# Optimization experiments

Hardware: AMD Instinct MI355X
Metric: run time of the kernel (lower is better)

## Reference

```python
import jax, jax.numpy as jnp
import numpy as np

NL, DM, DI, DS, DC, DR = 8, 512, 1024, 16, 4, 32  # layers, d_model, d_inner, d_state, d_conv, dt_rank
B_, F_, HW, PF, P = 8, 32, 160, 4, 16


def setup_inputs() -> dict:
    key = jax.random.key(0)
    ks = iter(jax.random.split(key, 64))
    def rn(shape, s=0.02):
        return jax.random.normal(next(ks), shape, jnp.float32) * s
    inp = {"x": jax.random.normal(next(ks), (B_, 1, F_, HW, HW), jnp.float32)}
    inp["patch_w"] = rn((P * P * PF * 1, DM)); inp["patch_b"] = jnp.zeros((DM,), jnp.float32)
    inp["in_proj_w"] = rn((NL, DM, 2 * DI))
    inp["conv_w"] = rn((NL, DI, DC), 0.2); inp["conv_b"] = jnp.zeros((NL, DI), jnp.float32)
    inp["xproj_w"] = rn((NL, DI, DR + 2 * DS))
    inp["dt_w"] = rn((NL, DR, DI)); inp["dt_bias"] = rn((NL, DI), 0.1)
    A0 = jnp.log(jnp.arange(1, DS + 1, dtype=jnp.float32))
    inp["A_log"] = jnp.tile(A0, (NL, DI, 1)); inp["D_skip"] = jnp.ones((NL, DI), jnp.float32)
    inp["conv_w_b"] = rn((NL, DI, DC), 0.2); inp["conv_b_b"] = jnp.zeros((NL, DI), jnp.float32)
    inp["xproj_w_b"] = rn((NL, DI, DR + 2 * DS))
    inp["dt_w_b"] = rn((NL, DR, DI)); inp["dt_bias_b"] = rn((NL, DI), 0.1)
    inp["A_log_b"] = jnp.tile(A0, (NL, DI, 1)); inp["D_skip_b"] = jnp.ones((NL, DI), jnp.float32)
    inp["out_proj_w"] = rn((NL, DI, DM))
    inp["ln1_g"] = jnp.ones((NL, DM), jnp.float32); inp["ln1_b"] = jnp.zeros((NL, DM), jnp.float32)
    inp["fc1_w"] = rn((NL, DM, 1024)); inp["fc1_b"] = jnp.zeros((NL, 1024), jnp.float32)
    inp["fc2_w"] = rn((NL, 1024, DM)); inp["fc2_b"] = jnp.zeros((NL, DM), jnp.float32)
    inp["ln2_g"] = jnp.ones((NL, DM), jnp.float32); inp["ln2_b"] = jnp.zeros((NL, DM), jnp.float32)
    return inp


def _ln(x, g, b):
    m = jnp.mean(x, -1, keepdims=True)
    v = jnp.mean(jnp.square(x - m), -1, keepdims=True)
    return (x - m) * jax.lax.rsqrt(v + 1e-5) * g + b


def _causal_conv(x, w, b):
    # x: (B, L, DI); depthwise causal conv over L, kernel DC, then SiLU
    xt = x.transpose(0, 2, 1)  # (B, DI, L)
    y = jax.lax.conv_general_dilated(xt, w[:, None, :], (1,), [(DC - 1, 0)],
                                     feature_group_count=DI,
                                     dimension_numbers=("NCH", "OIH", "NCH"))
    return jax.nn.silu(y + b[None, :, None]).transpose(0, 2, 1)


def _ssm(u, dt, A, Bm, Cm, Dv):
    # u, dt: (B, L, DI); A: (DI, DS); Bm, Cm: (B, L, DS); Dv: (DI,)
    def step(h, t):
        dt_t, B_t, C_t, u_t = t  # (B,DI),(B,DS),(B,DS),(B,DI)
        h = jnp.exp(dt_t[..., None] * A) * h + (dt_t * u_t)[..., None] * B_t[:, None, :]
        return h, jnp.einsum("bdn,bn->bd", h, C_t)
    h0 = jnp.zeros((u.shape[0], DI, DS), u.dtype)
    _, ys = jax.lax.scan(step, h0, (dt.swapaxes(0, 1), Bm.swapaxes(0, 1),
                                    Cm.swapaxes(0, 1), u.swapaxes(0, 1)))
    return ys.swapaxes(0, 1) + u * Dv


def _mamba_dir(xc, z, xp_w, dtw, dtb, a_log, dv):
    proj = xc @ xp_w  # (B, L, DR+2*DS)
    dti, Bm, Cm = jnp.split(proj, [DR, DR + DS], axis=-1)
    dt = jax.nn.softplus(dti @ dtw + dtb)
    y = _ssm(xc, dt, -jnp.exp(a_log), Bm, Cm, dv)
    return y * jax.nn.silu(z)


def reference(x, patch_w, patch_b, in_proj_w, conv_w, conv_b, xproj_w, dt_w, dt_bias,
              A_log, D_skip, conv_w_b, conv_b_b, xproj_w_b, dt_w_b, dt_bias_b,
              A_log_b, D_skip_b, out_proj_w, ln1_g, ln1_b, fc1_w, fc1_b,
              fc2_w, fc2_b, ln2_g, ln2_b):
    b, c, Ft, H, W = x.shape
    f, h, w = Ft // PF, H // P, W // P
    # Rearrange: b c (f pf) (h p1) (w p2) -> b (f h w) (p1 p2 pf c)
    xp = x.reshape(b, c, f, PF, h, P, w, P).transpose(0, 2, 4, 6, 5, 7, 3, 1)
    xt = xp.reshape(b, f * h * w, P * P * PF * c) @ patch_w + patch_b  # (B, 800, 512)
    outs = []
    for l in range(NL):
        xz = xt @ in_proj_w[l]
        xm, z = jnp.split(xz, 2, axis=-1)  # (B, L, DI) each
        yf = _mamba_dir(_causal_conv(xm, conv_w[l], conv_b[l]), z,
                        xproj_w[l], dt_w[l], dt_bias[l], A_log[l], D_skip[l])
        yb = _mamba_dir(_causal_conv(xm[:, ::-1], conv_w_b[l], conv_b_b[l]), z[:, ::-1],
                        xproj_w_b[l], dt_w_b[l], dt_bias_b[l], A_log_b[l], D_skip_b[l])
        y = (yf + yb[:, ::-1]) @ out_proj_w[l]
        xt = _ln(y, ln1_g[l], ln1_b[l]) + xt  # MambaLayer (dropout=eval identity) + residual
        m = jax.nn.gelu(xt @ fc1_w[l] + fc1_b[l], approximate=False) @ fc2_w[l] + fc2_b[l]
        xt = _ln(m, ln2_g[l], ln2_b[l]) + xt  # MlpChannel + residual
        outs.append(xt)
    return jnp.stack(outs)  # (NL, B, 800, 512); original returns this as a list
```

## Files before the change

### kernel.cpp

```cpp
#include <hip/hip_runtime.h>


typedef unsigned short u16;
typedef unsigned long long u64;
typedef short s16x8 __attribute__((ext_vector_type(8)));
typedef float f32x4 __attribute__((ext_vector_type(4)));

#define NSEG 10
#define SEGLEN 80

__device__ __forceinline__ float b2f(u16 u) {
    return __uint_as_float(((unsigned)u) << 16);
}
__device__ __forceinline__ u16 f2b(float f) {
    unsigned u = __float_as_uint(f);
    return (u16)((u + 0x7fffu + ((u >> 16) & 1u)) >> 16);
}
__device__ __forceinline__ float ldw(const void* p, size_t i, int bf) {
    return bf ? b2f(((const u16*)p)[i]) : ((const float*)p)[i];
}
__device__ __forceinline__ float4 ldw4(const void* p, size_t i, int bf) {
    if (bf) {
        ushort4 v = *(const ushort4*)((const u16*)p + i);
        return make_float4(b2f(v.x), b2f(v.y), b2f(v.z), b2f(v.w));
    }
    return *(const float4*)((const float*)p + i);
}

__device__ __forceinline__ int detect_bf(const void* w) {
    const u16* p = (const u16*)w;
    unsigned e = (p[threadIdx.x & 63] >> 7) & 0xFFu;
    u64 m = __ballot((e >= 0x60u) && (e <= 0x7Fu));
    return __popcll(m) >= 50 ? 1 : 0;
}

#if __has_builtin(__builtin_amdgcn_exp2f)
#define EXP2F(x) __builtin_amdgcn_exp2f(x)
#else
#define EXP2F(x) __expf((x) * 0.69314718055994531f)
#endif

template<int EPI>
__device__ __forceinline__ float epi_act(float x) {
    if (EPI == 2) {
        float t = __expf(-fabsf(x));
        return fmaxf(x, 0.f) + __logf(1.f + t);
    }
    if (EPI == 3) {
        float y = 0.7978845608f * fmaf(0.044715f * x, x * x, x);
        float e = __expf(fminf(2.f * y, 80.f));
        float th = (e - 1.f) / (e + 1.f);
        return 0.5f * x * (1.f + th);
    }
    return x;
}

__global__ __launch_bounds__(256) void transp_cvt(
    const void* __restrict__ src, u16* __restrict__ dst, int K, int N,
    const void* __restrict__ sniff)
{
    const int bf = detect_bf(sniff);
    __shared__ u16 tile[32][33];
    const int n0 = blockIdx.x * 32, k0 = blockIdx.y * 32;
    const size_t loff = (size_t)blockIdx.z * K * N;
    const int tx = threadIdx.x, ty = threadIdx.y;
    #pragma unroll
    for (int r = 0; r < 4; r++) {
        int ky = ty + r * 8;
        tile[ky][tx] = f2b(ldw(src, loff + (size_t)(k0 + ky) * N + n0 + tx, bf));
    }
    __syncthreads();
    #pragma unroll
    for (int r = 0; r < 4; r++) {
        int ny = ty + r * 8;
        dst[loff + (size_t)(n0 + ny) * K + k0 + tx] = tile[tx][ny];
    }
}

template<int EPI, bool OUTF, bool OUTB>
__global__ __launch_bounds__(256) void gemm_mfma(
    const u16* __restrict__ A, const u16* __restrict__ WT, size_t woff,
    const void* __restrict__ bias, size_t soff,
    float* __restrict__ Cf, u16* __restrict__ Cb,
    int M, int N, int K, const void* __restrict__ sniff)
{
    const int bf = detect_bf(sniff);
    __shared__ __align__(16) u16 As[128 * 32];
    __shared__ __align__(16) u16 Bs[128 * 32];
    const int tid = threadIdx.x;
    const int bm = blockIdx.y * 128, bn = blockIdx.x * 128;
    const int w = tid >> 6, lane = tid & 63;
    const int wm = (w >> 1) * 64, wn = (w & 1) * 64;
    const int lrow = lane & 15, q = lane >> 4;
    const u16* Wp = WT + woff;

    f32x4 acc[4][4];
    const f32x4 z4 = {0.f, 0.f, 0.f, 0.f};
    #pragma unroll
    for (int i = 0; i < 4; i++)
        #pragma unroll
        for (int j = 0; j < 4; j++) acc[i][j] = z4;

    for (int k0 = 0; k0 < K; k0 += 32) {
        if (k0) __syncthreads();
        #pragma unroll
        for (int c = 0; c < 2; c++) {
            int jj = tid + c * 256;
            int r = jj >> 2, kc = jj & 3;
            int kg = kc ^ ((r >> 1) & 3);
            int ra = bm + r; if (ra >= M) ra = M - 1;
            *(s16x8*)(As + r * 32 + kc * 8) =
                *(const s16x8*)(A + (size_t)ra * K + k0 + kg * 8);
            *(s16x8*)(Bs + r * 32 + kc * 8) =
                *(const s16x8*)(Wp + (size_t)(bn + r) * K + k0 + kg * 8);
        }
        __syncthreads();
        s16x8 af[4], bfr[4];
        #pragma unroll
        for (int mt = 0; mt < 4; mt++) {
            int m_ = wm + mt * 16 + lrow;
            af[mt] = *(const s16x8*)(As + m_ * 32 + ((q ^ ((m_ >> 1) & 3)) << 3));
        }
        #pragma unroll
        for (int nt = 0; nt < 4; nt++) {
            int n_ = wn + nt * 16 + lrow;
            bfr[nt] = *(const s16x8*)(Bs + n_ * 32 + ((q ^ ((n_ >> 1) & 3)) << 3));
        }
        #pragma unroll
        for (int mt = 0; mt < 4; mt++)
            #pragma unroll
            for (int nt = 0; nt < 4; nt++)
                acc[mt][nt] = __builtin_amdgcn_mfma_f32_16x16x32_bf16(
                    af[mt], bfr[nt], acc[mt][nt], 0, 0, 0);
    }

    float bv[4] = {0.f, 0.f, 0.f, 0.f};
    if (EPI >= 1) {
        #pragma unroll
        for (int nt = 0; nt < 4; nt++)
            bv[nt] = ldw(bias, soff + (size_t)(bn + wn + nt * 16 + lrow), bf);
    }
    #pragma unroll
    for (int mt = 0; mt < 4; mt++) {
        #pragma unroll
        for (int nt = 0; nt < 4; nt++) {
            int n = bn + wn + nt * 16 + lrow;
            #pragma unroll
            for (int reg = 0; reg < 4; reg++) {
                int m = bm + wm + mt * 16 + q * 4 + reg;
                if (m < M) {
                    float v = epi_act<EPI>(acc[mt][nt][reg] + bv[nt]);
                    if (OUTF) Cf[(size_t)m * N + n] = v;
                    if (OUTB) Cb[(size_t)m * N + n] = f2b(v);
                }
            }
        }
    }
}

template<int EPI>
__device__ __forceinline__ void gemm_body(
    const float* __restrict__ A,
    const void* __restrict__ Bw, size_t boff,
    const void* __restrict__ bias, size_t soff,
    float* __restrict__ C, int N, int K, int lda, int ldb, int ldc, int bf)
{
    __shared__ float As[16][68];
    __shared__ float Bs[16][68];
    const int tid = threadIdx.x;
    const int bm = blockIdx.y * 64;
    const int bn = blockIdx.x * 64;
    const int arow = tid >> 2, acol = (tid & 3) << 2;
    const int brow = tid >> 4, bcol = (tid & 15) << 2;
    const int ty = tid >> 4, tx = tid & 15;
    float acc[4][4] = {};

    const float* aptr = A + (size_t)(bm + arow) * lda + acol;
    const size_t bidx0 = boff + (size_t)brow * ldb + bn + bcol;

    for (int k0 = 0; k0 < K; k0 += 16) {
        float4 av = *(const float4*)(aptr + k0);
        float4 bvv = ldw4(Bw, bidx0 + (size_t)k0 * ldb, bf);
        As[acol + 0][arow] = av.x;
        As[acol + 1][arow] = av.y;
        As[acol + 2][arow] = av.z;
        As[acol + 3][arow] = av.w;
        Bs[brow][bcol + 0] = bvv.x;
        Bs[brow][bcol + 1] = bvv.y;
        Bs[brow][bcol + 2] = bvv.z;
        Bs[brow][bcol + 3] = bvv.w;
        __syncthreads();
        #pragma unroll
        for (int kk = 0; kk < 16; kk++) {
            float4 a4 = *(const float4*)&As[kk][ty << 2];
            float4 b4 = *(const float4*)&Bs[kk][tx << 2];
            float ar[4] = {a4.x, a4.y, a4.z, a4.w};
            float br[4] = {b4.x, b4.y, b4.z, b4.w};
            #pragma unroll
            for (int i = 0; i < 4; i++)
                #pragma unroll
                for (int j = 0; j < 4; j++)
                    acc[i][j] = fmaf(ar[i], br[j], acc[i][j]);
        }
        __syncthreads();
    }

    float bv4[4] = {0.f, 0.f, 0.f, 0.f};
    if (EPI >= 1) {
        float4 bb = ldw4(bias, soff + (size_t)(bn + (tx << 2)), bf);
        bv4[0] = bb.x; bv4[1] = bb.y; bv4[2] = bb.z; bv4[3] = bb.w;
    }
    #pragma unroll
    for (int i = 0; i < 4; i++) {
        float4 o;
        o.x = epi_act<EPI>(acc[i][0] + bv4[0]);
        o.y = epi_act<EPI>(acc[i][1] + bv4[1]);
        o.z = epi_act<EPI>(acc[i][2] + bv4[2]);
        o.w = epi_act<EPI>(acc[i][3] + bv4[3]);
        *(float4*)(C + (size_t)(bm + (ty << 2) + i) * ldc + bn + (tx << 2)) = o;
    }
}

template<int EPI>
__global__ __launch_bounds__(256) void gemm_dual(
    const float* __restrict__ A0, const float* __restrict__ A1,
    const void* __restrict__ Bw0, size_t boff0,
    const void* __restrict__ Bw1, size_t boff1,
    const void* __restrict__ bias0, size_t sof0,
    const void* __restrict__ bias1, size_t sof1,
    float* __restrict__ C0, float* __restrict__ C1,
    int N, int K, int lda, int ldb, int ldc,
    const void* __restrict__ sniff)
{
    const int bf = detect_bf(sniff);
    if (blockIdx.z == 0)
        gemm_body<EPI>(A0, Bw0, boff0, bias0, sof0, C0, N, K, lda, ldb, ldc, bf);
    else
        gemm_body<EPI>(A1, Bw1, boff1, bias1, sof1, C1, N, K, lda, ldb, ldc, bf);
}

__global__ __launch_bounds__(256) void xproj_splitk(
    const float* __restrict__ A0, const float* __restrict__ A1,
    const void* __restrict__ Bw0, size_t boff0,
    const void* __restrict__ Bw1, size_t boff1,
    float* __restrict__ P, int Mc, const void* __restrict__ sniff)
{
    const int bf = detect_bf(sniff);
    const int dir = blockIdx.z;
    const float* A = dir ? A1 : A0;
    const void* Bw = dir ? Bw1 : Bw0;
    const size_t boff = dir ? boff1 : boff0;

    __shared__ float As[16][68];
    __shared__ float Bs[16][68];
    const int tid = threadIdx.x;
    const int bm = blockIdx.y * 64;
    const int kbase = blockIdx.x * 128;
    const int arow = tid >> 2, acol = (tid & 3) << 2;
    const int brow = tid >> 4, bcol = (tid & 15) << 2;
    const int ty = tid >> 4, tx = tid & 15;
    float acc[4][4] = {};

    const float* aptr = A + (size_t)(bm + arow) * 1024 + kbase + acol;
    const size_t bidx0 = boff + (size_t)(kbase + brow) * 64 + bcol;

    for (int k0 = 0; k0 < 128; k0 += 16) {
        float4 av = *(const float4*)(aptr + k0);
        float4 bvv = ldw4(Bw, bidx0 + (size_t)k0 * 64, bf);
        As[acol + 0][arow] = av.x;
        As[acol + 1][arow] = av.y;
        As[acol + 2][arow] = av.z;
        As[acol + 3][arow] = av.w;
        Bs[brow][bcol + 0] = bvv.x;
        Bs[brow][bcol + 1] = bvv.y;
        Bs[brow][bcol + 2] = bvv.z;
        Bs[brow][bcol + 3] = bvv.w;
        __syncthreads();
        #pragma unroll
        for (int kk = 0; kk < 16; kk++) {
            float4 a4 = *(const float4*)&As[kk][ty << 2];
            float4 b4 = *(const float4*)&Bs[kk][tx << 2];
            float ar[4] = {a4.x, a4.y, a4.z, a4.w};
            float br[4] = {b4.x, b4.y, b4.z, b4.w};
            #pragma unroll
            for (int i = 0; i < 4; i++)
                #pragma unroll
                for (int j = 0; j < 4; j++)
                    acc[i][j] = fmaf(ar[i], br[j], acc[i][j]);
        }
        __syncthreads();
    }

    float* out = P + ((size_t)(blockIdx.x * 2 + dir) * Mc + bm) * 64;
    #pragma unroll
    for (int i = 0; i < 4; i++) {
        float4 o = {acc[i][0], acc[i][1], acc[i][2], acc[i][3]};
        *(float4*)(out + (size_t)((ty << 2) + i) * 64 + (tx << 2)) = o;
    }
}

__global__ __launch_bounds__(256) void xproj_reduce(
    const float* __restrict__ P, float* __restrict__ o0,
    float* __restrict__ o1, unsigned Md)
{
    const int dir = blockIdx.y;
    unsigned i = (blockIdx.x * 256 + threadIdx.x) * 4;
    const float* p = P + (size_t)dir * Md + i;
    float4 a = *(const float4*)p;
    #pragma unroll
    for (int kc = 1; kc < 8; kc++) {
        float4 bq = *(const float4*)(p + (size_t)kc * 2 * Md);
        a.x += bq.x; a.y += bq.y; a.z += bq.z; a.w += bq.w;
    }
    *(float4*)((dir ? o1 : o0) + i) = a;
}

__global__ __launch_bounds__(256) void im2col_patch(
    const void* __restrict__ x, size_t x0, u16* __restrict__ Pb,
    const void* __restrict__ sniff)
{
    const int bf = detect_bf(sniff);
    int idx = blockIdx.x * 256 + threadIdx.x;
    int p2 = idx & 15; int r = idx >> 4;
    int p1 = r & 15;  r >>= 4;
    int w = r % 10;   r /= 10;
    int h = r % 10;   r /= 10;
    int f = r & 7;    int b = r >> 3;
    int token = f * 100 + h * 10 + w;
    size_t xb = x0 + ((size_t)(b * 32 + f * 4) * 160 + h * 16 + p1) * 160
                   + (w * 16 + p2);
    ushort4 o;
    o.x = f2b(ldw(x, xb,         bf));
    o.y = f2b(ldw(x, xb + 25600, bf));
    o.z = f2b(ldw(x, xb + 51200, bf));
    o.w = f2b(ldw(x, xb + 76800, bf));
    *(ushort4*)(Pb + (size_t)(b * 800 + token) * 1024 + ((p1 * 16 + p2) << 2)) = o;
}

__global__ __launch_bounds__(256) void conv_dual(
    const float* __restrict__ xm,
    const void* __restrict__ cwF, size_t wFo,
    const void* __restrict__ cbF, size_t bFo,
    const void* __restrict__ cwB, size_t wBo,
    const void* __restrict__ cbB, size_t bBo,
    float* __restrict__ xcf, float* __restrict__ xcb,
    const void* __restrict__ sniff)
{
    const int bf = detect_bf(sniff);
    int idx = blockIdx.x * 256 + threadIdx.x;
    int d = idx & 1023;
    int bt = idx >> 10;
    int t = bt % 800, b = bt / 800;
    const float* base = xm + (size_t)b * 800 * 2048 + d;
    float v[7];
    #pragma unroll
    for (int j = 0; j < 7; j++) {
        int tt = t + j - 3;
        v[j] = (tt >= 0 && tt < 800) ? base[(size_t)tt * 2048] : 0.f;
    }
    float4 wf = ldw4(cwF, wFo + (size_t)d * 4, bf);
    float4 wb = ldw4(cwB, wBo + (size_t)d * 4, bf);
    float f = ldw(cbF, bFo + d, bf) + wf.x * v[0] + wf.y * v[1]
                                    + wf.z * v[2] + wf.w * v[3];
    float g = ldw(cbB, bBo + d, bf) + wb.x * v[6] + wb.y * v[5]
                                    + wb.z * v[4] + wb.w * v[3];
    xcf[(size_t)bt * 1024 + d] = f / (1.f + __expf(-f));
    xcb[(size_t)bt * 1024 + d] = g / (1.f + __expf(-g));
}

__device__ __forceinline__ float& scrf(float* s, unsigned i) {
    return s[(size_t)(i >> 10) * 2048 + (i & 1023)];
}

__device__ __forceinline__ void pow16(float q, float* e) {
    float q2 = q * q, q4 = q2 * q2, q8 = q4 * q4;
    e[0] = q;        e[1] = q2;       e[2] = q2 * q;   e[3] = q4;
    e[4] = q4 * q;   e[5] = q4 * q2;  e[6] = e[5] * q; e[7] = q8;
    e[8] = q8 * q;   e[9] = q8 * q2;  e[10] = e[9] * q; e[11] = q8 * q4;
    e[12] = e[11] * q; e[13] = e[11] * q2; e[14] = e[13] * q; e[15] = q8 * q8;
}

template<int DIR, int PASS, bool POW>
__device__ __forceinline__ void scan_seg_body(
    const float* u, const float* dt, const float* __restrict__ pr,
    const void* __restrict__ Al, size_t ao,
    const void* __restrict__ Dp, size_t dofs,
    float* y, float* scr, unsigned NSd, int b, int seg, int bf,
    float* lds)
{
    const int tid = threadIdx.x;
    const int d = blockIdx.x * 256 + tid;
    const long rb = (long)b * 800;
    constexpr int S = DIR ? -1 : 1;
    const int t0 = DIR ? 799 - seg * SEGLEN : seg * SEGLEN;

    for (int i = tid; i < 768; i += 256) {
        int tr = i >> 3, c4 = (i & 7) * 4;
        long tt = (long)t0 + (long)(S * tr);
        *(float4*)&lds[tr * 32 + c4] =
            *(const float4*)&pr[(rb + tt) * 64 + 32 + c4];
    }
    __syncthreads();

    float ac[16];
    #pragma unroll
    for (int n = 0; n < 16; n++)
        ac[n] = -__expf(ldw(Al, ao + (size_t)d * 16 + n, bf)) * 1.44269504f;
    const float ac0 = ac[0];
    const float Dv = (PASS == 3) ? ldw(Dp, dofs + d, bf) : 0.f;

    const unsigned sidx = ((unsigned)((b * 2 + DIR) * NSEG + seg) << 10) + d;
    float h[16];
    if (PASS == 3) {
        #pragma unroll
        for (int n = 0; n < 16; n++) h[n] = scrf(scr, (16 + n) * NSd + sidx);
    } else {
        #pragma unroll
        for (int n = 0; n < 16; n++) h[n] = 0.f;
    }
    float E[16]; float Q = 1.f;
    if (PASS == 1 && !POW) {
        #pragma unroll
        for (int n = 0; n < 16; n++) E[n] = 1.f;
    }

    const float* pdt = dt + (rb + t0) * 1024 + d;
    const float* pu  = u  + (rb + t0) * 1024 + d;
    float*       py  = y  + (rb + t0) * 1024 + d;

    float dA[8], uA[8], dB[8], uB_[8];
    #pragma unroll
    for (int j = 0; j < 8; j++) { dA[j] = pdt[S * j * 1024]; uA[j] = pu[S * j * 1024]; }
    pdt += S * 8192; pu += S * 8192;

    for (int it = 0; it < SEGLEN / 8; it++) {
        #pragma unroll
        for (int j = 0; j < 8; j++) { dB[j] = pdt[S * j * 1024]; uB_[j] = pu[S * j * 1024]; }
        pdt += S * 8192; pu += S * 8192;

        #pragma unroll
        for (int j = 0; j < 8; j++) {
            const float dtv = dA[j], uv = uA[j];
            const float du = dtv * uv;
            float e[16];
            if (POW) {
                float q = EXP2F(dtv * ac0);
                pow16(q, e);
                if (PASS == 1) Q *= q;
            } else {
                #pragma unroll
                for (int n = 0; n < 16; n++) e[n] = EXP2F(dtv * ac[n]);
                if (PASS == 1) {
                    #pragma unroll
                    for (int n = 0; n < 16; n++) E[n] *= e[n];
                }
            }
            const float* bcp = lds + (it * 8 + j) * 32;
            float bs[16];
            *(float4*)&bs[0]  = *(const float4*)&bcp[0];
            *(float4*)&bs[4]  = *(const float4*)&bcp[4];
            *(float4*)&bs[8]  = *(const float4*)&bcp[8];
            *(float4*)&bs[12] = *(const float4*)&bcp[12];
            #pragma unroll
            for (int n = 0; n < 16; n++) h[n] = e[n] * h[n] + du * bs[n];
            if (PASS == 3) {
                float cs[16];
                *(float4*)&cs[0]  = *(const float4*)&bcp[16];
                *(float4*)&cs[4]  = *(const float4*)&bcp[20];
                *(float4*)&cs[8]  = *(const float4*)&bcp[24];
                *(float4*)&cs[12] = *(const float4*)&bcp[28];
                float s0 = 0.f, s1 = 0.f, s2 = 0.f, s3 = 0.f;
                #pragma unroll
                for (int n = 0; n < 4; n++) {
                    s0 = fmaf(h[n],      cs[n],      s0);
                    s1 = fmaf(h[4 + n],  cs[4 + n],  s1);
                    s2 = fmaf(h[8 + n],  cs[8 + n],  s2);
                    s3 = fmaf(h[12 + n], cs[12 + n], s3);
                }
                py[S * j * 1024] = fmaf(uv, Dv, (s0 + s1) + (s2 + s3));
            }
        }
        if (PASS == 3) py += S * 8192;
        #pragma unroll
        for (int j = 0; j < 8; j++) { dA[j] = dB[j]; uA[j] = uB_[j]; }
    }

    if (PASS == 1) {
        if (POW) pow16(Q, E);
        #pragma unroll
        for (int n = 0; n < 16; n++) {
            scrf(scr, n * NSd + sidx)        = E[n];
            scrf(scr, (16 + n) * NSd + sidx) = h[n];
        }
    }
}

template<int PASS>
__global__ __launch_bounds__(256) void ssm_seg(
    const float* uF, const float* dtF, const float* __restrict__ pF,
    const float* uB, const float* dtB, const float* __restrict__ pB,
    const void* __restrict__ AlF, const void* __restrict__ AlB, size_t ao,
    const void* __restrict__ DF,  const void* __restrict__ DB,  size_t dofs,
    float* yF, float* yB, float* scr, unsigned NSd,
    const void* __restrict__ sniff)
{
    __shared__ float lds[96 * 32];
    const int bf = detect_bf(sniff);
    const int b = blockIdx.y;
    const int z = blockIdx.z;
    const int dir = z >= NSEG ? 1 : 0;
    const int seg = dir ? z - NSEG : z;
    const int d = blockIdx.x * 256 + threadIdx.x;

    const void* Al = dir ? AlB : AlF;
    float m0 = __expf(ldw(Al, ao + (size_t)d * 16 + 0, bf));
    bool okb = true;
    #pragma unroll
    for (int n = 1; n < 16; n++) {
        float mn = __expf(ldw(Al, ao + (size_t)d * 16 + n, bf));
        okb &= fabsf(mn - (n + 1) * m0) <= 1e-3f * (n + 1) * m0;
    }
    const bool ok = __all(okb) != 0;

    if (dir == 0) {
        if (ok) scan_seg_body<0, PASS, true >(uF, dtF, pF, AlF, ao, DF, dofs,
                                              yF, scr, NSd, b, seg, bf, lds);
        else    scan_seg_body<0, PASS, false>(uF, dtF, pF, AlF, ao, DF, dofs,
                                              yF, scr, NSd, b, seg, bf, lds);
    } else {
        if (ok) scan_seg_body<1, PASS, true >(uB, dtB, pB, AlB, ao, DB, dofs,
                                              yB, scr, NSd, b, seg, bf, lds);
        else    scan_seg_body<1, PASS, false>(uB, dtB, pB, AlB, ao, DB, dofs,
                                              yB, scr, NSd, b, seg, bf, lds);
    }
}

__global__ __launch_bounds__(256) void ssm_comb(float* scr, unsigned NSd)
{
    int idx = blockIdx.x * 256 + threadIdx.x;
    int d = idx & 1023;
    int n = (idx >> 10) & 15;
    int bdir = idx >> 14;
    float h = 0.f;
    for (int s = 0; s < NSEG; s++) {
        unsigned sidx = ((unsigned)(bdir * NSEG + s) << 10) + d;
        float Ev = scrf(scr, n * NSd + sidx);
        float He = scrf(scr, (16 + n) * NSd + sidx);
        scrf(scr, (16 + n) * NSd + sidx) = h;
        h = Ev * h + He;
    }
}

__global__ __launch_bounds__(256) void addcvt(
    const float* __restrict__ a, const float* __restrict__ b,
    const float* __restrict__ z, u16* __restrict__ o)
{
    int i = (blockIdx.x * 256 + threadIdx.x) * 4;
    int t = i >> 10, d = i & 1023;
    float4 va = *(const float4*)(a + i);
    float4 vb = *(const float4*)(b + i);
    float4 vz = *(const float4*)(z + (size_t)t * 2048 + 1024 + d);
    float s0 = vz.x / (1.f + __expf(-vz.x));
    float s1 = vz.y / (1.f + __expf(-vz.y));
    float s2 = vz.z / (1.f + __expf(-vz.z));
    float s3 = vz.w / (1.f + __expf(-vz.w));
    ushort4 r;
    r.x = f2b((va.x + vb.x) * s0); r.y = f2b((va.y + vb.y) * s1);
    r.z = f2b((va.z + vb.z) * s2); r.w = f2b((va.w + vb.w) * s3);
    *(ushort4*)(o + i) = r;
}

__global__ __launch_bounds__(256) void ln_residual(
    const float* __restrict__ Y, const void* __restrict__ g, size_t go,
    const void* __restrict__ bb, size_t bo,
    float* __restrict__ XT, u16* __restrict__ XTb, float* __restrict__ out,
    const void* __restrict__ sniff)
{
    const int bf = detect_bf(sniff);
    int wv = threadIdx.x >> 6, lane = threadIdx.x & 63;
    int token = blockIdx.x * 4 + wv;
    const float* y = Y + (size_t)token * 512;
    float v[8], s = 0.f, s2 = 0.f;
    #pragma unroll
    for (int j = 0; j < 8; j++) {
        v[j] = y[lane + j * 64];
        s += v[j]; s2 += v[j] * v[j];
    }
    #pragma unroll
    for (int off = 32; off >= 1; off >>= 1) {
        s  += __shfl_xor(s,  off, 64);
        s2 += __shfl_xor(s2, off, 64);
    }
    float mean = s * (1.f / 512.f);
    float var  = s2 * (1.f / 512.f) - mean * mean;
    float rs = rsqrtf(var + 1e-5f);
    float* xt = XT + (size_t)token * 512;
    #pragma unroll
    for (int j = 0; j < 8; j++) {
        int c = lane + j * 64;
        float val = (v[j] - mean) * rs * ldw(g, go + c, bf)
                  + ldw(bb, bo + c, bf) + xt[c];
        xt[c] = val;
        XTb[(size_t)token * 512 + c] = f2b(val);
        if (out) out[(size_t)token * 512 + c] = val;
    }
}

extern "C" void kernel_launch(void* const* d_in, const int* in_sizes, int n_in,
                              void* d_out, int out_size, void* d_ws, size_t ws_size,
                              hipStream_t stream)
{
    (void)in_sizes; (void)n_in; (void)out_size;
    const void* X      = d_in[0];
    const void* patchW = d_in[1];
    const void* patchB = d_in[2];
    const void* inW    = d_in[3];
    const void* convW  = d_in[4];
    const void* convBi = d_in[5];
    const void* xprojW = d_in[6];
    const void* dtW    = d_in[7];
    const void* dtBias = d_in[8];
    const void* Alog   = d_in[9];
    const void* Dsk    = d_in[10];
    const void* convWb = d_in[11];
    const void* convBb = d_in[12];
    const void* xprojWb= d_in[13];
    const void* dtWb   = d_in[14];
    const void* dtBiasb= d_in[15];
    const void* Alogb  = d_in[16];
    const void* Dskb   = d_in[17];
    const void* outW   = d_in[18];
    const void* ln1g   = d_in[19];
    const void* ln1b   = d_in[20];
    const void* fc1W   = d_in[21];
    const void* fc1B   = d_in[22];
    const void* fc2W   = d_in[23];
    const void* fc2B   = d_in[24];
    const void* ln2g   = d_in[25];
    const void* ln2b   = d_in[26];
    const void* SN     = patchW;

    const size_t IN_OFF  = 524288;
    const size_t OUT_OFF = 8912896;
    const size_t FC1_OFF = 13107200;
    const size_t FC2_OFF = 17301504;
    const size_t WB_FLOATS = 10747904;

    int nc = 1;
    auto need = [&](int Mc) {
        return (WB_FLOATS + (size_t)Mc * 8064 + 16384) * 4;
    };
    if (need(6400) > ws_size) nc = 2;
    if (need(3200) > ws_size) nc = 4;
    const int bc = 8 / nc;
    const int Mc = bc * 800;
    const int GY = Mc / 64;
    const int GYM = (Mc + 127) / 128;
    const unsigned NSd = (unsigned)bc * 2 * NSEG * 1024;

    u16* WB = (u16*)d_ws;
    float* cur = (float*)d_ws + WB_FLOATS;
    float* XT  = cur;              cur += (size_t)Mc * 512;
    u16*  XTb  = (u16*)cur;        cur += (size_t)Mc * 256;
    float* XZ  = cur;              cur += (size_t)Mc * 2048;
    float* XCF = cur;              cur += (size_t)Mc * 1024;
    float* XCB = cur;              cur += (size_t)Mc * 1024;
    float* PRF = cur;              cur += (size_t)Mc * 64;
    float* PRB = cur;              cur += (size_t)Mc * 64;
    float* DTF = cur;              cur += (size_t)Mc * 1024;
    float* DTB = cur;              cur += (size_t)Mc * 1024;
    u16*  M1b  = (u16*)cur;        cur += (size_t)Mc * 512;
    u16*  YSb  = (u16*)cur;        cur += (size_t)Mc * 512;
    u16*  PATCHb = (u16*)XCF;
    float* YO  = XZ;
    float* M2  = XZ + (size_t)Mc * 512;

    transp_cvt<<<dim3(16, 32, 1), dim3(32, 8), 0, stream>>>(patchW, WB, 1024, 512, SN);
    transp_cvt<<<dim3(64, 16, 8), dim3(32, 8), 0, stream>>>(inW,  WB + IN_OFF, 512, 2048, SN);
    transp_cvt<<<dim3(16, 32, 8), dim3(32, 8), 0, stream>>>(outW, WB + OUT_OFF, 1024, 512, SN);
    transp_cvt<<<dim3(32, 16, 8), dim3(32, 8), 0, stream>>>(fc1W, WB + FC1_OFF, 512, 1024, SN);
    transp_cvt<<<dim3(16, 32, 8), dim3(32, 8), 0, stream>>>(fc2W, WB + FC2_OFF, 1024, 512, SN);

    for (int c = 0; c < nc; c++) {
        const size_t x0 = (size_t)c * bc * 819200;

        im2col_patch<<<Mc, 256, 0, stream>>>(X, x0, PATCHb, SN);
        gemm_mfma<1, true, true><<<dim3(4, GYM), 256, 0, stream>>>(
            PATCHb, WB, 0, patchB, 0, XT, XTb, Mc, 512, 1024, SN);

        for (int l = 0; l < 8; l++) {
            gemm_mfma<0, true, false><<<dim3(16, GYM), 256, 0, stream>>>(
                XTb, WB, IN_OFF + (size_t)l * 1048576, nullptr, 0,
                XZ, nullptr, Mc, 2048, 512, SN);
            conv_dual<<<Mc * 4, 256, 0, stream>>>(
                XZ, convW, (size_t)l * 4096, convBi, (size_t)l * 1024,
                convWb, (size_t)l * 4096, convBb, (size_t)l * 1024,
                XCF, XCB, SN);
            xproj_splitk<<<dim3(8, GY, 2), 256, 0, stream>>>(
                XCF, XCB, xprojW, (size_t)l * 65536, xprojWb, (size_t)l * 65536,
                DTF, Mc, SN);
            xproj_reduce<<<dim3(Mc / 16, 2), 256, 0, stream>>>(
                DTF, PRF, PRB, (unsigned)Mc * 64);
            gemm_dual<2><<<dim3(16, GY, 2), 256, 0, stream>>>(
                PRF, PRB, dtW, (size_t)l * 32768, dtWb, (size_t)l * 32768,
                dtBias, (size_t)l * 1024, dtBiasb, (size_t)l * 1024,
                DTF, DTB, 1024, 32, 64, 1024, 1024, SN);
            ssm_seg<1><<<dim3(4, bc, 2 * NSEG), 256, 0, stream>>>(
                XCF, DTF, PRF, XCB, DTB, PRB,
                Alog, Alogb, (size_t)l * 16384,
                Dsk, Dskb, (size_t)l * 1024,
                XCF, XCB, XZ, NSd, SN);
            ssm_comb<<<bc * 128, 256, 0, stream>>>(XZ, NSd);
            ssm_seg<3><<<dim3(4, bc, 2 * NSEG), 256, 0, stream>>>(
                XCF, DTF, PRF, XCB, DTB, PRB,
                Alog, Alogb, (size_t)l * 16384,
                Dsk, Dskb, (size_t)l * 1024,
                XCF, XCB, XZ, NSd, SN);
            addcvt<<<Mc, 256, 0, stream>>>(XCF, XCB, XZ, YSb);
            gemm_mfma<0, true, false><<<dim3(4, GYM), 256, 0, stream>>>(
                YSb, WB, OUT_OFF + (size_t)l * 524288, nullptr, 0,
                YO, nullptr, Mc, 512, 1024, SN);
            ln_residual<<<Mc / 4, 256, 0, stream>>>(
                YO, ln1g, (size_t)l * 512, ln1b, (size_t)l * 512,
                XT, XTb, nullptr, SN);
            gemm_mfma<3, false, true><<<dim3(8, GYM), 256, 0, stream>>>(
                XTb, WB, FC1_OFF + (size_t)l * 524288, fc1B, (size_t)l * 1024,
                nullptr, M1b, Mc, 1024, 512, SN);
            gemm_mfma<1, true, false><<<dim3(4, GYM), 256, 0, stream>>>(
                M1b, WB, FC2_OFF + (size_t)l * 524288, fc2B, (size_t)l * 512,
                M2, nullptr, Mc, 512, 1024, SN);
            ln_residual<<<Mc / 4, 256, 0, stream>>>(
                M2, ln2g, (size_t)l * 512, ln2b, (size_t)l * 512,
                XT, XTb,
                (float*)d_out + (size_t)l * 3276800 + (size_t)c * Mc * 512, SN);
        }
    }
}
```

Measured before the change: 3.099 ms.

## Double scan segments, store carry states in bf16, derive decay from dt sum

Splits each sequence into 20 segments of 40 steps instead of 10 of 80, doubling the blocks in the chunked selective scan. The per-segment decay is now computed once from the accumulated dt rather than multiplied step by step. Segment carry states and decays are stored as bf16 in the scratch buffer to halve that traffic. This adds more sequential combine work and bf16 rounding error in the carried states, which may affect accuracy.

Measured after the change: 3.065 ms. About the same (-1.1%).

```diff
diff --git a/kernel.cpp b/kernel.cpp
--- a/kernel.cpp
+++ b/kernel.cpp
@@ -6,8 +6,8 @@
 typedef short s16x8 __attribute__((ext_vector_type(8)));
 typedef float f32x4 __attribute__((ext_vector_type(4)));
 
-#define NSEG 10
-#define SEGLEN 80
+#define NSEG 20
+#define SEGLEN 40
 
 __device__ __forceinline__ float b2f(u16 u) {
     return __uint_as_float(((unsigned)u) << 16);
@@ -368,8 +368,8 @@
     xcb[(size_t)bt * 1024 + d] = g / (1.f + __expf(-g));
 }
 
-__device__ __forceinline__ float& scrf(float* s, unsigned i) {
-    return s[(size_t)(i >> 10) * 2048 + (i & 1023)];
+__device__ __forceinline__ u16& scrh(u16* s, unsigned i) {
+    return s[(size_t)(i >> 11) * 4096 + (i & 2047)];
 }
 
 __device__ __forceinline__ void pow16(float q, float* e) {
@@ -385,7 +385,7 @@
     const float* u, const float* dt, const float* __restrict__ pr,
     const void* __restrict__ Al, size_t ao,
     const void* __restrict__ Dp, size_t dofs,
-    float* y, float* scr, unsigned NSd, int b, int seg, int bf,
+    float* y, u16* scr, unsigned NSd, int b, int seg, int bf,
     float* lds)
 {
     const int tid = threadIdx.x;
@@ -394,7 +394,7 @@
     constexpr int S = DIR ? -1 : 1;
     const int t0 = DIR ? 799 - seg * SEGLEN : seg * SEGLEN;
 
-    for (int i = tid; i < 768; i += 256) {
+    for (int i = tid; i < SEGLEN * 8; i += 256) {
         int tr = i >> 3, c4 = (i & 7) * 4;
         long tt = (long)t0 + (long)(S * tr);
         *(float4*)&lds[tr * 32 + c4] =
@@ -413,16 +413,12 @@
     float h[16];
     if (PASS == 3) {
         #pragma unroll
-        for (int n = 0; n < 16; n++) h[n] = scrf(scr, (16 + n) * NSd + sidx);
+        for (int n = 0; n < 16; n++) h[n] = b2f(scrh(scr, (16 + n) * NSd + sidx));
     } else {
         #pragma unroll
         for (int n = 0; n < 16; n++) h[n] = 0.f;
     }
-    float E[16]; float Q = 1.f;
-    if (PASS == 1 && !POW) {
-        #pragma unroll
-        for (int n = 0; n < 16; n++) E[n] = 1.f;
-    }
+    float dtsum = 0.f;
 
     const float* pdt = dt + (rb + t0) * 1024 + d;
     const float* pu  = u  + (rb + t0) * 1024 + d;
@@ -442,18 +438,14 @@
         for (int j = 0; j < 8; j++) {
             const float dtv = dA[j], uv = uA[j];
             const float du = dtv * uv;
+            if (PASS == 1) dtsum += dtv;
             float e[16];
             if (POW) {
                 float q = EXP2F(dtv * ac0);
                 pow16(q, e);
-                if (PASS == 1) Q *= q;
             } else {
                 #pragma unroll
                 for (int n = 0; n < 16; n++) e[n] = EXP2F(dtv * ac[n]);
-                if (PASS == 1) {
-                    #pragma unroll
-                    for (int n = 0; n < 16; n++) E[n] *= e[n];
-                }
             }
             const float* bcp = lds + (it * 8 + j) * 32;
             float bs[16];
@@ -486,11 +478,17 @@
     }
 
     if (PASS == 1) {
-        if (POW) pow16(Q, E);
+        float E[16];
+        if (POW) {
+            pow16(EXP2F(dtsum * ac0), E);
+        } else {
+            #pragma unroll
+            for (int n = 0; n < 16; n++) E[n] = EXP2F(dtsum * ac[n]);
+        }
         #pragma unroll
         for (int n = 0; n < 16; n++) {
-            scrf(scr, n * NSd + sidx)        = E[n];
-            scrf(scr, (16 + n) * NSd + sidx) = h[n];
+            scrh(scr, n * NSd + sidx)        = f2b(E[n]);
+            scrh(scr, (16 + n) * NSd + sidx) = f2b(h[n]);
         }
     }
 }
@@ -501,10 +499,10 @@
     const float* uB, const float* dtB, const float* __restrict__ pB,
     const void* __restrict__ AlF, const void* __restrict__ AlB, size_t ao,
     const void* __restrict__ DF,  const void* __restrict__ DB,  size_t dofs,
-    float* yF, float* yB, float* scr, unsigned NSd,
+    float* yF, float* yB, u16* scr, unsigned NSd,
     const void* __restrict__ sniff)
 {
-    __shared__ float lds[96 * 32];
+    __shared__ float lds[SEGLEN * 32];
     const int bf = detect_bf(sniff);
     const int b = blockIdx.y;
     const int z = blockIdx.z;
@@ -535,7 +533,7 @@
     }
 }
 
-__global__ __launch_bounds__(256) void ssm_comb(float* scr, unsigned NSd)
+__global__ __launch_bounds__(256) void ssm_comb(u16* scr, unsigned NSd)
 {
     int idx = blockIdx.x * 256 + threadIdx.x;
     int d = idx & 1023;
@@ -544,9 +542,9 @@
     float h = 0.f;
     for (int s = 0; s < NSEG; s++) {
         unsigned sidx = ((unsigned)(bdir * NSEG + s) << 10) + d;
-        float Ev = scrf(scr, n * NSd + sidx);
-        float He = scrf(scr, (16 + n) * NSd + sidx);
-        scrf(scr, (16 + n) * NSd + sidx) = h;
+        float Ev = b2f(scrh(scr, n * NSd + sidx));
+        float He = b2f(scrh(scr, (16 + n) * NSd + sidx));
+        scrh(scr, (16 + n) * NSd + sidx) = f2b(h);
         h = Ev * h + He;
     }
 }
@@ -709,13 +707,13 @@
                 XCF, DTF, PRF, XCB, DTB, PRB,
                 Alog, Alogb, (size_t)l * 16384,
                 Dsk, Dskb, (size_t)l * 1024,
-                XCF, XCB, XZ, NSd, SN);
-            ssm_comb<<<bc * 128, 256, 0, stream>>>(XZ, NSd);
+                XCF, XCB, (u16*)XZ, NSd, SN);
+            ssm_comb<<<bc * 128, 256, 0, stream>>>((u16*)XZ, NSd);
             ssm_seg<3><<<dim3(4, bc, 2 * NSEG), 256, 0, stream>>>(
                 XCF, DTF, PRF, XCB, DTB, PRB,
                 Alog, Alogb, (size_t)l * 16384,
                 Dsk, Dskb, (size_t)l * 1024,
-                XCF, XCB, XZ, NSd, SN);
+                XCF, XCB, (u16*)XZ, NSd, SN);
             addcvt<<<Mc, 256, 0, stream>>>(XCF, XCB, XZ, YSb);
             gemm_mfma<0, true, false><<<dim3(4, GYM), 256, 0, stream>>>(
                 YSb, WB, OUT_OFF + (size_t)l * 524288, nullptr, 0,
```
